# Kernel optimization log

Measured on AMD Instinct MI355X. Metric: run time of the kernel, lower is better.

The kernel has to match this reference:

```python
import jax, jax.numpy as jnp
import numpy as np

EPS = 1e-07
GAMMA = 2.0
LAMBDA_DISCO = 1000.0


def _binary_entropy(target, output):
    x = jnp.clip(output, EPS, 1.0 - EPS)
    return -target * jnp.log(x) - (1.0 - target) * jnp.log(1.0 - x)


def _focal_bce(target, output, y_class, y_pred_class):
    yc = y_class[:, 0]
    ypc = y_pred_class[:, 0]
    y_pred = output[:, 0]
    bce = _binary_entropy(target, y_pred)
    m = jnp.mean(ypc)
    s = jnp.std(ypc)  # population std, matches tf.math.reduce_std
    norm = jnp.clip((ypc - m) / (2.0 * s) + 0.5, 0.0, 1.0)
    class_weight_factor = ((1.0 - yc) * norm) ** GAMMA
    norm_factor = jnp.sum(1.0 - yc) / jnp.sum(class_weight_factor)
    return class_weight_factor * bce * norm_factor


def _distance_corr(var_1, var_2, w, power):
    # pairwise |x_i - x_j| distance matrices [N, N]
    amat = jnp.abs(var_1[:, None] - var_1[None, :])
    bmat = jnp.abs(var_2[:, None] - var_2[None, :])
    amatavg = jnp.mean(amat * w, axis=1)
    bmatavg = jnp.mean(bmat * w, axis=1)
    # double centering (tile layout: minuend_1[i,j]=avg[j], minuend_2[i,j]=avg[i])
    Amat = amat - amatavg[None, :] - amatavg[:, None] + jnp.mean(amatavg * w)
    Bmat = bmat - bmatavg[None, :] - bmatavg[:, None] + jnp.mean(bmatavg * w)
    ABavg = jnp.abs(jnp.mean(Amat * Bmat * w, axis=1))
    AAavg = jnp.mean(Amat * Amat * w, axis=1)
    BBavg = jnp.mean(Bmat * Bmat * w, axis=1)
    mAB = jnp.mean(ABavg * w)
    mAA = jnp.mean(AAavg * w)
    mBB = jnp.mean(BBavg * w)
    if power == 1:
        dCorr = mAB / jnp.sqrt(jnp.abs(mAA * mBB) + 1e-12)
    elif power == 2:
        dCorr = mAB ** 2 / (jnp.abs(mAA * mBB) + 1e-12)
    else:
        dCorr = (mAB / jnp.sqrt(mAA * mBB) + 1e-12) ** power
    dCorr = jnp.where(jnp.isnan(dCorr), 0.0, dCorr)
    dCorr = jnp.where(dCorr < 0.0, 0.0, dCorr)
    return dCorr


def setup_inputs() -> dict:
    N = 4096
    key = jax.random.key(0)
    ks = jax.random.split(key, 6)
    target = jnp.round(jax.random.uniform(ks[0], (N,), dtype=jnp.float32))
    output = jax.random.uniform(ks[1], (N, 1), dtype=jnp.float32, minval=0.02, maxval=0.98)
    y_class = jnp.round(jax.random.uniform(ks[2], (N, 1), dtype=jnp.float32))
    y_pred_class = jax.random.uniform(ks[3], (N, 1), dtype=jnp.float32, minval=0.02, maxval=0.98)
    var_1 = jax.random.normal(ks[4], (N,), dtype=jnp.float32) * 20.0 + 100.0  # mass-like
    var_2 = jax.random.uniform(ks[5], (N,), dtype=jnp.float32)  # classifier-output-like
    normedweight = jnp.ones((N,), dtype=jnp.float32)  # sums to N as required
    return {"target": target, "output": output, "y_class": y_class,
            "y_pred_class": y_pred_class, "var_1": var_1, "var_2": var_2,
            "normedweight": normedweight, "power": 1}


def reference(target, output, y_class, y_pred_class, var_1, var_2, normedweight, power):
    focal = _focal_bce(target, output, y_class, y_pred_class)
    dcorr = _distance_corr(var_1, var_2, normedweight, power)
    return jnp.mean(focal) + LAMBDA_DISCO * dcorr
```

## Files before the change

kernel.cpp:

```cpp
#include <hip/hip_runtime.h>
#include <math.h>

#define N 4096
#define RPB 16
#define LANES 16
#define NBLK (N / RPB)
#define HALF 2048
#define FEPS 1e-7f


__device__ __forceinline__ double block_reduce(double v) {
    __shared__ double buf[4];
    int tid = threadIdx.x;
    #pragma unroll
    for (int o = 32; o > 0; o >>= 1) v += __shfl_down(v, o, 64);
    __syncthreads();
    if ((tid & 63) == 0) buf[tid >> 6] = v;
    __syncthreads();
    return buf[0] + buf[1] + buf[2] + buf[3];
}

__global__ __launch_bounds__(256) void k1(
        const float* __restrict__ target,
        const float* __restrict__ output,
        const float* __restrict__ y_class,
        const float* __restrict__ y_pred_class,
        const float* __restrict__ v1,
        const float* __restrict__ v2,
        const float* __restrict__ w,
        double* __restrict__ wd,
        int* __restrict__ counter,
        float* __restrict__ rowA,
        float* __restrict__ rowB) {
    int tid = threadIdx.x;
    int b = blockIdx.x;

    if (b == NBLK) {
        if (tid == 0) *counter = 0;
        double s_ypc = 0.0, s_ypc2 = 0.0, s_yc = 0.0;
        for (int i = tid; i < N; i += 256) {
            float ypc = y_pred_class[i];
            s_ypc  += (double)ypc;
            s_ypc2 += (double)ypc * (double)ypc;
            s_yc   += (double)y_class[i];
        }
        double t_ypc  = block_reduce(s_ypc);
        double t_ypc2 = block_reduce(s_ypc2);
        double t_yc   = block_reduce(s_yc);

        __shared__ float  sm, sinv2s;
        __shared__ double s_sum1myc;
        if (tid == 0) {
            double m   = t_ypc / (double)N;
            double var = t_ypc2 / (double)N - m * m;
            double sd  = sqrt(var > 0.0 ? var : 0.0);
            sm     = (float)m;
            sinv2s = (float)(1.0 / (2.0 * sd));
            s_sum1myc = (double)N - t_yc;
        }
        __syncthreads();

        float m = sm, inv2s = sinv2s;
        double s_cwf = 0.0, s_cwfb = 0.0;
        for (int i = tid; i < N; i += 256) {
            float yc  = y_class[i];
            float ypc = y_pred_class[i];
            float nrm = (ypc - m) * inv2s + 0.5f;
            nrm = fminf(fmaxf(nrm, 0.0f), 1.0f);
            float c1  = (1.0f - yc) * nrm;
            float cwf = c1 * c1;
            float x = fminf(fmaxf(output[i], FEPS), 1.0f - FEPS);
            float t = target[i];
            float bce = -t * logf(x) - (1.0f - t) * logf(1.0f - x);
            s_cwf  += (double)cwf;
            s_cwfb += (double)cwf * (double)bce;
        }
        double t_cwf  = block_reduce(s_cwf);
        double t_cwfb = block_reduce(s_cwfb);
        if (tid == 0) wd[0] = t_cwfb * (s_sum1myc / t_cwf) / (double)N;
        return;
    }

    __shared__ float s1[N], s2[N], sw[N];
    #pragma unroll
    for (int i = tid * 4; i < N; i += 1024) {
        *(float4*)&s1[i] = *(const float4*)&v1[i];
        *(float4*)&s2[i] = *(const float4*)&v2[i];
        *(float4*)&sw[i] = *(const float4*)&w [i];
    }
    __syncthreads();

    int lane16 = tid & (LANES - 1);
    int r      = tid >> 4;
    int i      = b * RPB + r;
    float a  = s1[i];
    float bb = s2[i];
    float sa = 0.0f, sb = 0.0f;
    #pragma unroll 8
    for (int k = 0; k < N / (LANES * 4); ++k) {
        int j = 4 * lane16 + 64 * k;
        float4 x1 = *(const float4*)&s1[j];
        float4 x2 = *(const float4*)&s2[j];
        float4 xw = *(const float4*)&sw[j];
        sa = fmaf(fabsf(a - x1.x), xw.x, sa);
        sa = fmaf(fabsf(a - x1.y), xw.y, sa);
        sa = fmaf(fabsf(a - x1.z), xw.z, sa);
        sa = fmaf(fabsf(a - x1.w), xw.w, sa);
        sb = fmaf(fabsf(bb - x2.x), xw.x, sb);
        sb = fmaf(fabsf(bb - x2.y), xw.y, sb);
        sb = fmaf(fabsf(bb - x2.z), xw.z, sb);
        sb = fmaf(fabsf(bb - x2.w), xw.w, sb);
    }
    #pragma unroll
    for (int o = 1; o < LANES; o <<= 1) {
        sa += __shfl_xor(sa, o, LANES);
        sb += __shfl_xor(sb, o, LANES);
    }
    if (lane16 == 0) { rowA[i] = sa; rowB[i] = sb; }
}

__global__ __launch_bounds__(256) void k2(
        const float* __restrict__ v1,
        const float* __restrict__ v2,
        const float* __restrict__ w,
        const float* __restrict__ rowA,
        const float* __restrict__ rowB,
        const double* __restrict__ wd,
        const int* __restrict__ power,
        int* __restrict__ counter,
        double* __restrict__ pAB,
        double* __restrict__ pAA,
        double* __restrict__ pBB,
        float* __restrict__ out) {
    __shared__ float s1[HALF], s2[HALF], sw[HALF], sav[HALF], sbv[HALF];
    __shared__ double rAB[RPB], rAA[RPB], rBB[RPB];
    int tid = threadIdx.x;
    int b = blockIdx.x;
    const float invN = 1.0f / (float)N;

    double sgA = 0.0, sgB = 0.0;
    for (int i = tid; i < N; i += 256) {
        double wi = (double)w[i];
        sgA += (double)rowA[i] * wi;
        sgB += (double)rowB[i] * wi;
    }
    const double NN = (double)N * (double)N;
    float gA = (float)(block_reduce(sgA) / NN);
    float gB = (float)(block_reduce(sgB) / NN);

    int lane16 = tid & (LANES - 1);
    int r      = tid >> 4;
    int i      = b * RPB + r;
    float a  = v1[i];
    float bb = v2[i];
    float cA = rowA[i] * invN - gA;
    float cB = rowB[i] * invN - gB;

    float ab = 0.0f, aa = 0.0f, bbs = 0.0f;
    for (int h = 0; h < 2; ++h) {
        int j0 = h * HALF;
        __syncthreads();
        #pragma unroll
        for (int t = tid * 4; t < HALF; t += 1024) {
            *(float4*)&s1[t] = *(const float4*)&v1[j0 + t];
            *(float4*)&s2[t] = *(const float4*)&v2[j0 + t];
            *(float4*)&sw[t] = *(const float4*)&w [j0 + t];
            float4 ra = *(const float4*)&rowA[j0 + t];
            float4 rb = *(const float4*)&rowB[j0 + t];
            ra.x *= invN; ra.y *= invN; ra.z *= invN; ra.w *= invN;
            rb.x *= invN; rb.y *= invN; rb.z *= invN; rb.w *= invN;
            *(float4*)&sav[t] = ra;
            *(float4*)&sbv[t] = rb;
        }
        __syncthreads();
        #pragma unroll 4
        for (int k = 0; k < HALF / (LANES * 4); ++k) {
            int j = 4 * lane16 + 64 * k;
            float4 x1 = *(const float4*)&s1[j];
            float4 x2 = *(const float4*)&s2[j];
            float4 xw = *(const float4*)&sw[j];
            float4 xa = *(const float4*)&sav[j];
            float4 xb = *(const float4*)&sbv[j];
            #define STEP(c)                                              \
            {                                                            \
                float Am = fabsf(a  - x1.c) - xa.c - cA;                 \
                float Bm = fabsf(bb - x2.c) - xb.c - cB;                 \
                float Amw = Am * xw.c;                                   \
                ab  = fmaf(Amw, Bm, ab);                                 \
                aa  = fmaf(Amw, Am, aa);                                 \
                bbs = fmaf(Bm * xw.c, Bm, bbs);                          \
            }
            STEP(x) STEP(y) STEP(z) STEP(w)
            #undef STEP
        }
    }
    #pragma unroll
    for (int o = 1; o < LANES; o <<= 1) {
        ab  += __shfl_xor(ab,  o, LANES);
        aa  += __shfl_xor(aa,  o, LANES);
        bbs += __shfl_xor(bbs, o, LANES);
    }
    if (lane16 == 0) {
        double wi = (double)w[i];
        rAB[r] = fabs((double)ab) * wi;
        rAA[r] = (double)aa * wi;
        rBB[r] = (double)bbs * wi;
    }
    __syncthreads();
    if (tid == 0) {
        double tab = 0.0, taa = 0.0, tbb = 0.0;
        #pragma unroll
        for (int q = 0; q < RPB; ++q) { tab += rAB[q]; taa += rAA[q]; tbb += rBB[q]; }
        pAB[b] = tab; pAA[b] = taa; pBB[b] = tbb;
    }

    __shared__ int isLast;
    if (tid == 0) {
        __threadfence();
        int old = atomicAdd(counter, 1);
        isLast = (old == NBLK - 1);
    }
    __syncthreads();
    if (!isLast) return;
    __threadfence();

    double vab = pAB[tid], vaa = pAA[tid], vbb = pBB[tid];
    double tab = block_reduce(vab);
    double taa = block_reduce(vaa);
    double tbb = block_reduce(vbb);
    if (tid == 0) {
        const double NN2 = (double)N * (double)N;
        double mAB = tab / NN2;
        double mAA = taa / NN2;
        double mBB = tbb / NN2;
        int p = power[0];
        double d;
        if (p == 1) {
            d = mAB / sqrt(fabs(mAA * mBB) + 1e-12);
        } else if (p == 2) {
            d = (mAB * mAB) / (fabs(mAA * mBB) + 1e-12);
        } else {
            d = pow(mAB / sqrt(mAA * mBB) + 1e-12, (double)p);
        }
        if (isnan(d)) d = 0.0;
        if (d < 0.0)  d = 0.0;
        out[0] = (float)(wd[0] + 1000.0 * d);
    }
}

extern "C" void kernel_launch(void* const* d_in, const int* in_sizes, int n_in,
                              void* d_out, int out_size, void* d_ws, size_t ws_size,
                              hipStream_t stream) {
    const float* target       = (const float*)d_in[0];
    const float* output       = (const float*)d_in[1];
    const float* y_class      = (const float*)d_in[2];
    const float* y_pred_class = (const float*)d_in[3];
    const float* var_1        = (const float*)d_in[4];
    const float* var_2        = (const float*)d_in[5];
    const float* normedweight = (const float*)d_in[6];
    const int*   power        = (const int*)d_in[7];
    float* out = (float*)d_out;

    char*   ws      = (char*)d_ws;
    double* wd      = (double*)ws;
    int*    counter = (int*)(ws + 16);
    double* pAB     = (double*)(ws + 64);
    double* pAA     = pAB + NBLK;
    double* pBB     = pAA + NBLK;
    float*  rowA    = (float*)(pBB + NBLK);
    float*  rowB    = rowA + N;

    k1<<<NBLK + 1, 256, 0, stream>>>(target, output, y_class, y_pred_class,
                                     var_1, var_2, normedweight, wd, counter, rowA, rowB);
    k2<<<NBLK, 256, 0, stream>>>(var_1, var_2, normedweight, rowA, rowB,
                                 wd, power, counter, pAB, pAA, pBB, out);
}
```

Baseline: 37.03 us.

## Split column range across block pairs and compute two rows per thread group

```diff
diff --git a/kernel.cpp b/kernel.cpp
--- a/kernel.cpp
+++ b/kernel.cpp
@@ -2,10 +2,11 @@
 #include <math.h>
 
 #define N 4096
-#define RPB 16
+#define HALF 2048
+#define RPB 32
 #define LANES 16
-#define NBLK (N / RPB)
-#define HALF 2048
+#define NRB (N / RPB)
+#define NPASS (NRB * 2)
 #define FEPS 1e-7f
 
 
@@ -30,12 +31,12 @@
         const float* __restrict__ w,
         double* __restrict__ wd,
         int* __restrict__ counter,
-        float* __restrict__ rowA,
-        float* __restrict__ rowB) {
+        float* __restrict__ rowA_p,
+        float* __restrict__ rowB_p) {
     int tid = threadIdx.x;
     int b = blockIdx.x;
 
-    if (b == NBLK) {
+    if (b == NPASS) {
         if (tid == 0) *counter = 0;
         double s_ypc = 0.0, s_ypc2 = 0.0, s_yc = 0.0;
         for (int i = tid; i < N; i += 256) {
@@ -81,158 +82,183 @@
         return;
     }
 
-    __shared__ float s1[N], s2[N], sw[N];
-    #pragma unroll
-    for (int i = tid * 4; i < N; i += 1024) {
-        *(float4*)&s1[i] = *(const float4*)&v1[i];
-        *(float4*)&s2[i] = *(const float4*)&v2[i];
-        *(float4*)&sw[i] = *(const float4*)&w [i];
-    }
-    __syncthreads();
-
-    int lane16 = tid & (LANES - 1);
-    int r      = tid >> 4;
-    int i      = b * RPB + r;
-    float a  = s1[i];
-    float bb = s2[i];
-    float sa = 0.0f, sb = 0.0f;
+    int h  = b & 1;
+    int rb = b >> 1;
+    int j0 = h * HALF;
+    __shared__ float s1[HALF], s2[HALF], sw[HALF];
+    for (int t = tid * 4; t < HALF; t += 1024) {
+        *(float4*)&s1[t] = *(const float4*)&v1[j0 + t];
+        *(float4*)&s2[t] = *(const float4*)&v2[j0 + t];
+        *(float4*)&sw[t] = *(const float4*)&w [j0 + t];
+    }
+    __syncthreads();
+
+    int lane = tid & (LANES - 1);
+    int g    = tid >> 4;
+    int i0   = rb * RPB + g * 2;
+    float a0 = v1[i0],     a1 = v1[i0 + 1];
+    float b0 = v2[i0],     b1 = v2[i0 + 1];
+    float sa0 = 0.f, sa1 = 0.f, sb0 = 0.f, sb1 = 0.f;
     #pragma unroll 8
-    for (int k = 0; k < N / (LANES * 4); ++k) {
-        int j = 4 * lane16 + 64 * k;
+    for (int k = 0; k < HALF / (LANES * 4); ++k) {
+        int j = 4 * lane + 64 * k;
         float4 x1 = *(const float4*)&s1[j];
         float4 x2 = *(const float4*)&s2[j];
         float4 xw = *(const float4*)&sw[j];
-        sa = fmaf(fabsf(a - x1.x), xw.x, sa);
-        sa = fmaf(fabsf(a - x1.y), xw.y, sa);
-        sa = fmaf(fabsf(a - x1.z), xw.z, sa);
-        sa = fmaf(fabsf(a - x1.w), xw.w, sa);
-        sb = fmaf(fabsf(bb - x2.x), xw.x, sb);
-        sb = fmaf(fabsf(bb - x2.y), xw.y, sb);
-        sb = fmaf(fabsf(bb - x2.z), xw.z, sb);
-        sb = fmaf(fabsf(bb - x2.w), xw.w, sb);
+        #define P1(c)                                  \
+        {                                              \
+            sa0 = fmaf(fabsf(a0 - x1.c), xw.c, sa0);   \
+            sa1 = fmaf(fabsf(a1 - x1.c), xw.c, sa1);   \
+            sb0 = fmaf(fabsf(b0 - x2.c), xw.c, sb0);   \
+            sb1 = fmaf(fabsf(b1 - x2.c), xw.c, sb1);   \
+        }
+        P1(x) P1(y) P1(z) P1(w)
+        #undef P1
     }
     #pragma unroll
     for (int o = 1; o < LANES; o <<= 1) {
-        sa += __shfl_xor(sa, o, LANES);
-        sb += __shfl_xor(sb, o, LANES);
-    }
-    if (lane16 == 0) { rowA[i] = sa; rowB[i] = sb; }
+        sa0 += __shfl_xor(sa0, o, LANES);
+        sa1 += __shfl_xor(sa1, o, LANES);
+        sb0 += __shfl_xor(sb0, o, LANES);
+        sb1 += __shfl_xor(sb1, o, LANES);
+    }
+    if (lane == 0) {
+        rowA_p[h * N + i0]     = sa0;
+        rowA_p[h * N + i0 + 1] = sa1;
+        rowB_p[h * N + i0]     = sb0;
+        rowB_p[h * N + i0 + 1] = sb1;
+    }
 }
 
 __global__ __launch_bounds__(256) void k2(
         const float* __restrict__ v1,
         const float* __restrict__ v2,
         const float* __restrict__ w,
-        const float* __restrict__ rowA,
-        const float* __restrict__ rowB,
+        const float* __restrict__ rowA_p,
+        const float* __restrict__ rowB_p,
         const double* __restrict__ wd,
         const int* __restrict__ power,
         int* __restrict__ counter,
-        double* __restrict__ pAB,
-        double* __restrict__ pAA,
-        double* __restrict__ pBB,
+        float* __restrict__ pABr,
+        float* __restrict__ pAAr,
+        float* __restrict__ pBBr,
         float* __restrict__ out) {
     __shared__ float s1[HALF], s2[HALF], sw[HALF], sav[HALF], sbv[HALF];
-    __shared__ double rAB[RPB], rAA[RPB], rBB[RPB];
     int tid = threadIdx.x;
     int b = blockIdx.x;
+    int h  = b & 1;
+    int rb = b >> 1;
+    int j0 = h * HALF;
     const float invN = 1.0f / (float)N;
+
+    for (int t = tid * 4; t < HALF; t += 1024) {
+        *(float4*)&s1[t] = *(const float4*)&v1[j0 + t];
+        *(float4*)&s2[t] = *(const float4*)&v2[j0 + t];
+        *(float4*)&sw[t] = *(const float4*)&w [j0 + t];
+        float4 r0 = *(const float4*)&rowA_p[j0 + t];
+        float4 r1 = *(const float4*)&rowA_p[N + j0 + t];
+        float4 q0 = *(const float4*)&rowB_p[j0 + t];
+        float4 q1 = *(const float4*)&rowB_p[N + j0 + t];
+        float4 ra, rbv;
+        ra.x  = (r0.x + r1.x) * invN;  ra.y  = (r0.y + r1.y) * invN;
+        ra.z  = (r0.z + r1.z) * invN;  ra.w  = (r0.w + r1.w) * invN;
+        rbv.x = (q0.x + q1.x) * invN;  rbv.y = (q0.y + q1.y) * invN;
+        rbv.z = (q0.z + q1.z) * invN;  rbv.w = (q0.w + q1.w) * invN;
+        *(float4*)&sav[t] = ra;
+        *(float4*)&sbv[t] = rbv;
+    }
+    __syncthreads();
 
     double sgA = 0.0, sgB = 0.0;
     for (int i = tid; i < N; i += 256) {
         double wi = (double)w[i];
-        sgA += (double)rowA[i] * wi;
-        sgB += (double)rowB[i] * wi;
+        sgA += (double)(rowA_p[i] + rowA_p[N + i]) * wi;
+        sgB += (double)(rowB_p[i] + rowB_p[N + i]) * wi;
     }
     const double NN = (double)N * (double)N;
     float gA = (float)(block_reduce(sgA) / NN);
     float gB = (float)(block_reduce(sgB) / NN);
 
-    int lane16 = tid & (LANES - 1);
-    int r      = tid >> 4;
-    int i      = b * RPB + r;
-    float a  = v1[i];
-    float bb = v2[i];
-    float cA = rowA[i] * invN - gA;
-    float cB = rowB[i] * invN - gB;
-
-    float ab = 0.0f, aa = 0.0f, bbs = 0.0f;
-    for (int h = 0; h < 2; ++h) {
-        int j0 = h * HALF;
-        __syncthreads();
-        #pragma unroll
-        for (int t = tid * 4; t < HALF; t += 1024) {
-            *(float4*)&s1[t] = *(const float4*)&v1[j0 + t];
-            *(float4*)&s2[t] = *(const float4*)&v2[j0 + t];
-            *(float4*)&sw[t] = *(const float4*)&w [j0 + t];
-            float4 ra = *(const float4*)&rowA[j0 + t];
-            float4 rb = *(const float4*)&rowB[j0 + t];
-            ra.x *= invN; ra.y *= invN; ra.z *= invN; ra.w *= invN;
-            rb.x *= invN; rb.y *= invN; rb.z *= invN; rb.w *= invN;
-            *(float4*)&sav[t] = ra;
-            *(float4*)&sbv[t] = rb;
-        }
-        __syncthreads();
-        #pragma unroll 4
-        for (int k = 0; k < HALF / (LANES * 4); ++k) {
-            int j = 4 * lane16 + 64 * k;
-            float4 x1 = *(const float4*)&s1[j];
-            float4 x2 = *(const float4*)&s2[j];
-            float4 xw = *(const float4*)&sw[j];
-            float4 xa = *(const float4*)&sav[j];
-            float4 xb = *(const float4*)&sbv[j];
-            #define STEP(c)                                              \
-            {                                                            \
-                float Am = fabsf(a  - x1.c) - xa.c - cA;                 \
-                float Bm = fabsf(bb - x2.c) - xb.c - cB;                 \
-                float Amw = Am * xw.c;                                   \
-                ab  = fmaf(Amw, Bm, ab);                                 \
-                aa  = fmaf(Amw, Am, aa);                                 \
-                bbs = fmaf(Bm * xw.c, Bm, bbs);                          \
-            }
-            STEP(x) STEP(y) STEP(z) STEP(w)
-            #undef STEP
-        }
+    int lane = tid & (LANES - 1);
+    int g    = tid >> 4;
+    int i0   = rb * RPB + g * 2;
+    float a0 = v1[i0],   a1 = v1[i0 + 1];
+    float e0 = v2[i0],   e1 = v2[i0 + 1];
+    float cA0 = (rowA_p[i0]     + rowA_p[N + i0])     * invN - gA;
+    float cA1 = (rowA_p[i0 + 1] + rowA_p[N + i0 + 1]) * invN - gA;
+    float cB0 = (rowB_p[i0]     + rowB_p[N + i0])     * invN - gB;
+    float cB1 = (rowB_p[i0 + 1] + rowB_p[N + i0 + 1]) * invN - gB;
+
+    float ab0 = 0.f, aa0 = 0.f, bb0 = 0.f;
+    float ab1 = 0.f, aa1 = 0.f, bb1 = 0.f;
+    #pragma unroll 4
+    for (int k = 0; k < HALF / (LANES * 4); ++k) {
+        int j = 4 * lane + 64 * k;
+        float4 x1 = *(const float4*)&s1[j];
+        float4 x2 = *(const float4*)&s2[j];
+        float4 xw = *(const float4*)&sw[j];
+        float4 xa = *(const float4*)&sav[j];
+        float4 xb = *(const float4*)&sbv[j];
+        #define P2(c)                                            \
+        {                                                        \
+            float Am0 = fabsf(a0 - x1.c) - xa.c - cA0;           \
+            float Bm0 = fabsf(e0 - x2.c) - xb.c - cB0;           \
+            float Am1 = fabsf(a1 - x1.c) - xa.c - cA1;           \
+            float Bm1 = fabsf(e1 - x2.c) - xb.c - cB1;           \
+            float Aw0 = Am0 * xw.c, Bw0 = Bm0 * xw.c;            \
+            float Aw1 = Am1 * xw.c, Bw1 = Bm1 * xw.c;            \
+            ab0 = fmaf(Aw0, Bm0, ab0);                           \
+            aa0 = fmaf(Aw0, Am0, aa0);                           \
+            bb0 = fmaf(Bw0, Bm0, bb0);                           \
+            ab1 = fmaf(Aw1, Bm1, ab1);                           \
+            aa1 = fmaf(Aw1, Am1, aa1);                           \
+            bb1 = fmaf(Bw1, Bm1, bb1);                           \
+        }
+        P2(x) P2(y) P2(z) P2(w)
+        #undef P2
     }
     #pragma unroll
     for (int o = 1; o < LANES; o <<= 1) {
-        ab  += __shfl_xor(ab,  o, LANES);
-        aa  += __shfl_xor(aa,  o, LANES);
-        bbs += __shfl_xor(bbs, o, LANES);
-    }
-    if (lane16 == 0) {
-        double wi = (double)w[i];
-        rAB[r] = fabs((double)ab) * wi;
-        rAA[r] = (double)aa * wi;
-        rBB[r] = (double)bbs * wi;
-    }
-    __syncthreads();
-    if (tid == 0) {
-        double tab = 0.0, taa = 0.0, tbb = 0.0;
-        #pragma unroll
-        for (int q = 0; q < RPB; ++q) { tab += rAB[q]; taa += rAA[q]; tbb += rBB[q]; }
-        pAB[b] = tab; pAA[b] = taa; pBB[b] = tbb;
+        ab0 += __shfl_xor(ab0, o, LANES);
+        aa0 += __shfl_xor(aa0, o, LANES);
+        bb0 += __shfl_xor(bb0, o, LANES);
+        ab1 += __shfl_xor(ab1, o, LANES);
+        aa1 += __shfl_xor(aa1, o, LANES);
+        bb1 += __shfl_xor(bb1, o, LANES);
+    }
+    if (lane == 0) {
+        pABr[h * N + i0]     = ab0;
+        pABr[h * N + i0 + 1] = ab1;
+        pAAr[h * N + i0]     = aa0;
+        pAAr[h * N + i0 + 1] = aa1;
+        pBBr[h * N + i0]     = bb0;
+        pBBr[h * N + i0 + 1] = bb1;
     }
 
     __shared__ int isLast;
     if (tid == 0) {
         __threadfence();
         int old = atomicAdd(counter, 1);
-        isLast = (old == NBLK - 1);
+        isLast = (old == NPASS - 1);
     }
     __syncthreads();
     if (!isLast) return;
     __threadfence();
 
-    double vab = pAB[tid], vaa = pAA[tid], vbb = pBB[tid];
-    double tab = block_reduce(vab);
-    double taa = block_reduce(vaa);
-    double tbb = block_reduce(vbb);
+    double sab = 0.0, saa = 0.0, sbb = 0.0;
+    for (int i = tid; i < N; i += 256) {
+        double wi = (double)w[i];
+        sab += fabs((double)(pABr[i] + pABr[N + i])) * wi;
+        saa += (double)(pAAr[i] + pAAr[N + i]) * wi;
+        sbb += (double)(pBBr[i] + pBBr[N + i]) * wi;
+    }
+    double tab = block_reduce(sab);
+    double taa = block_reduce(saa);
+    double tbb = block_reduce(sbb);
     if (tid == 0) {
-        const double NN2 = (double)N * (double)N;
-        double mAB = tab / NN2;
-        double mAA = taa / NN2;
-        double mBB = tbb / NN2;
+        double mAB = tab / NN;
+        double mAA = taa / NN;
+        double mBB = tbb / NN;
         int p = power[0];
         double d;
         if (p == 1) {
@@ -264,14 +290,15 @@
     char*   ws      = (char*)d_ws;
     double* wd      = (double*)ws;
     int*    counter = (int*)(ws + 16);
-    double* pAB     = (double*)(ws + 64);
-    double* pAA     = pAB + NBLK;
-    double* pBB     = pAA + NBLK;
-    float*  rowA    = (float*)(pBB + NBLK);
-    float*  rowB    = rowA + N;
-
-    k1<<<NBLK + 1, 256, 0, stream>>>(target, output, y_class, y_pred_class,
-                                     var_1, var_2, normedweight, wd, counter, rowA, rowB);
-    k2<<<NBLK, 256, 0, stream>>>(var_1, var_2, normedweight, rowA, rowB,
-                                 wd, power, counter, pAB, pAA, pBB, out);
+    float*  rowA_p  = (float*)(ws + 64);
+    float*  rowB_p  = rowA_p + 2 * N;
+    float*  pABr    = rowB_p + 2 * N;
+    float*  pAAr    = pABr  + 2 * N;
+    float*  pBBr    = pAAr  + 2 * N;
+
+    k1<<<NPASS + 1, 256, 0, stream>>>(target, output, y_class, y_pred_class,
+                                      var_1, var_2, normedweight, wd, counter,
+                                      rowA_p, rowB_p);
+    k2<<<NPASS, 256, 0, stream>>>(var_1, var_2, normedweight, rowA_p, rowB_p,
+                                  wd, power, counter, pABr, pAAr, pBBr, out);
 }
```

After: 39.47 us. 6.6% more time.
